# Optimization experiments

Hardware: AMD Instinct MI355X
Metric: run time of the kernel (lower is better)

## Reference

```python
import jax, jax.numpy as jnp
import numpy as np

HIDDEN = 128
IN_SIZE = 1
OUT_SIZE = 1
ENC_T = 8192
DEC_T = 4096


def _lstm_step(h, c, x, Wih, Whh, bih, bhh):
    # PyTorch LSTM gate order: i, f, g, o
    gates = Wih @ x + Whh @ h + bih + bhh  # [4H]
    i, f, g, o = jnp.split(gates, 4)
    c = jax.nn.sigmoid(f) * c + jax.nn.sigmoid(i) * jnp.tanh(g)
    h = jax.nn.sigmoid(o) * jnp.tanh(c)
    return h, c


def setup_inputs() -> dict:
    key = jax.random.key(0)
    ks = jax.random.split(key, 12)
    k = 1.0 / np.sqrt(HIDDEN)  # PyTorch default init bound
    u = lambda kk, shape: jax.random.uniform(kk, shape, jnp.float32, -k, k)
    return {
        "input_seq": jax.random.normal(ks[0], (ENC_T,), jnp.float32),
        "enc_Wih": u(ks[1], (4 * HIDDEN, IN_SIZE)),
        "enc_Whh": u(ks[2], (4 * HIDDEN, HIDDEN)),
        "enc_bih": u(ks[3], (4 * HIDDEN,)),
        "enc_bhh": u(ks[4], (4 * HIDDEN,)),
        "dec_Wih": u(ks[5], (4 * HIDDEN, OUT_SIZE)),
        "dec_Whh": u(ks[6], (4 * HIDDEN, HIDDEN)),
        "dec_bih": u(ks[7], (4 * HIDDEN,)),
        "dec_bhh": u(ks[8], (4 * HIDDEN,)),
        "fc_W": u(ks[9], (OUT_SIZE, HIDDEN)),
        "fc_b": u(ks[10], (OUT_SIZE,)),
        "target_seq_len": DEC_T,
    }


def reference(input_seq, enc_Wih, enc_Whh, enc_bih, enc_bhh,
              dec_Wih, dec_Whh, dec_bih, dec_bhh, fc_W, fc_b,
              target_seq_len):
    H = enc_Whh.shape[1]
    dt = input_seq.dtype

    def enc_step(carry, xt):
        h, c = carry
        h, c = _lstm_step(h, c, xt[None], enc_Wih, enc_Whh, enc_bih, enc_bhh)
        return (h, c), None

    (h, c), _ = jax.lax.scan(enc_step,
                             (jnp.zeros(H, dt), jnp.zeros(H, dt)),
                             input_seq)

    def dec_step(carry, _):
        h, c, y = carry  # y: previous prediction, shape [1]
        h, c = _lstm_step(h, c, y, dec_Wih, dec_Whh, dec_bih, dec_bhh)
        pred = fc_W @ h + fc_b  # [1]
        return (h, c, pred), pred

    _, preds = jax.lax.scan(dec_step, (h, c, jnp.zeros(1, dt)),
                            None, length=target_seq_len)
    # preds: [T_out, 1] -> torch.cat(outputs, dim=1) gives [1, T_out]
    return preds.T
```

## Files before the change

### kernel.cpp

```cpp
#include <hip/hip_runtime.h>


#define H      128
#define ENC_T  8192
#define DEC_T  4096
#define NT     512
#define NBLK   1
#define PBUF   5120

#define LOG2E  1.4426950408889634f

typedef float v2f __attribute__((ext_vector_type(2)));

__device__ __forceinline__ v2f pk_fma_s(v2f a, v2f b_sgpr, v2f c) {
    v2f d;
    asm("v_pk_fma_f32 %0, %1, %2, %3" : "=v"(d) : "v"(a), "s"(b_sgpr), "v"(c));
    return d;
}
__device__ __forceinline__ v2f pk_mul_s(v2f a, v2f b_sgpr) {
    v2f d;
    asm("v_pk_mul_f32 %0, %1, %2" : "=v"(d) : "v"(a), "s"(b_sgpr));
    return d;
}
__device__ __forceinline__ v2f pk_fma(v2f a, v2f b, v2f c) {
    v2f d;
    asm("v_pk_fma_f32 %0, %1, %2, %3" : "=v"(d) : "v"(a), "v"(b), "v"(c));
    return d;
}
__device__ __forceinline__ float exp2fast(float x) {
    float d;
    asm("v_exp_f32 %0, %1" : "=v"(d) : "v"(x));
    return d;
}
__device__ __forceinline__ float tanhfast(float x) {
    const float e = exp2fast(2.0f * LOG2E * x);
    return fmaf(-2.0f, __builtin_amdgcn_rcpf(1.0f + e), 1.0f);
}
__device__ __forceinline__ float rdlane(float v, int l) {
    return __int_as_float(__builtin_amdgcn_readlane(__float_as_int(v), l));
}
template <int CTRL>
__device__ __forceinline__ float qperm(float v) {
    return __int_as_float(
        __builtin_amdgcn_mov_dpp(__float_as_int(v), CTRL, 0xf, 0xf, true));
}

__global__ __launch_bounds__(NT, 2)
void seq2seq_lstm(const float* __restrict__ input_seq,
                  const float* __restrict__ enc_Wih,
                  const float* __restrict__ enc_Whh,
                  const float* __restrict__ enc_bih,
                  const float* __restrict__ enc_bhh,
                  const float* __restrict__ dec_Wih,
                  const float* __restrict__ dec_Whh,
                  const float* __restrict__ dec_bih,
                  const float* __restrict__ dec_bhh,
                  const float* __restrict__ fc_W,
                  const float* __restrict__ fc_b,
                  float* __restrict__ out,
                  unsigned* __restrict__ wsflag)
{
    (void)wsflag;
    __shared__ __align__(16) float xin[ENC_T];
    __shared__ __align__(16) float hbuf[2][H];
    __shared__ __align__(16) float part[2][PBUF];

    const int t    = threadIdx.x;
    const int lane = t & 63;
    const int wv   = t >> 6;
    const int jb   = 16 * wv;
    const int qq   = lane >> 2;
    const int g    = lane & 3;
    const int myu  = jb + qq;
    const int myrow = g * H + myu;

    const int rbase = 80 * wv + 16 * g + qq;
    const int wbase = 640 * wv + 80 * (lane >> 4) + (lane & 15);

    const float sA  = (g == 2) ? 1.0f : 0.0f;
    const float sB  = (g == 2) ? -2.0f : 1.0f;
    const float sS2 = ((g == 2) ? 2.0f : -1.0f) * LOG2E;

    {
        const float4* s = (const float4*)input_seq;
        float4* d = (float4*)xin;
        for (int i = t; i < ENC_T / 4; i += NT) d[i] = s[i];
    }

    v2f w2[8][8];
#pragma unroll
    for (int s = 0; s < 8; ++s) {
        const v2f* Wr = (const v2f*)(enc_Whh + (64 * s + lane) * H + jb);
#pragma unroll
        for (int jj = 0; jj < 8; ++jj) w2[s][jj] = Wr[jj];
    }
    float bias_r = enc_bih[myrow] + enc_bhh[myrow];
    float wih_r  = enc_Wih[myrow];

    float cst = 0.f;
    float hn  = 0.f;
    __syncthreads();

#define MATVEC(PB)                                                          \
    {                                                                       \
        v2f acc2[8];                                                        \
        {                          \
            const float se = rdlane(hn, 3);                                 \
            const float so = rdlane(hn, 7);                                 \
            const v2f hp = {se, so};                                        \
            _Pragma("unroll") for (int s = 0; s < 8; ++s)                   \
                acc2[s] = pk_mul_s(w2[s][0], hp);                           \
        }                                                                   \
        _Pragma("unroll") for (int jj = 1; jj < 8; ++jj) {                  \
            const float se = rdlane(hn, 8 * jj + 3);                        \
            const float so = rdlane(hn, 8 * jj + 7);                        \
            const v2f hp = {se, so};                                        \
            _Pragma("unroll") for (int s = 0; s < 8; ++s)                   \
                acc2[s] = pk_fma_s(w2[s][jj], hp, acc2[s]);                 \
        }                                                                   \
        float* pb_ = &part[PB][wbase];                                      \
        pb_[0]   = acc2[0].x + acc2[0].y;                                   \
        pb_[320] = acc2[1].x + acc2[1].y;                                   \
        pb_[16]  = acc2[2].x + acc2[2].y;                                   \
        pb_[336] = acc2[3].x + acc2[3].y;                                   \
        pb_[32]  = acc2[4].x + acc2[4].y;                                   \
        pb_[352] = acc2[5].x + acc2[5].y;                                   \
        pb_[48]  = acc2[6].x + acc2[6].y;                                   \
        pb_[368] = acc2[7].x + acc2[7].y;                                   \
    }

#define RED_LOAD(PB)                                                        \
    const float* rb_ = &part[PB][rbase];                                    \
    const float r0_ = rb_[0],    r1_ = rb_[640],  r2_ = rb_[1280],          \
                r3_ = rb_[1920], r4_ = rb_[2560], r5_ = rb_[3200],          \
                r6_ = rb_[3840], r7_ = rb_[4480];

#define RED_FIN(PB, ABASE, STH)                                             \
    {                                                                       \
        const float a = (ABASE) + (((r0_ + r1_) + (r2_ + r3_)) +            \
                                   ((r4_ + r5_) + (r6_ + r7_)));            \
        const float e = exp2fast(sS2 * a);                                  \
        const float r = __builtin_amdgcn_rcpf(1.0f + e);                    \
        const float v = fmaf(sB, r, sA);                                    \
        const float vi = qperm<0x00>(v);                   \
        const float vf = qperm<0x55>(v);                   \
        const float vg = qperm<0xAA>(v);                   \
        const float vo = qperm<0xFF>(v);                   \
        cst = fmaf(vf, cst, vi * vg);                                       \
        hn  = vo * tanhfast(cst);                                           \
        if (STH && g == 3) hbuf[PB][myu] = hn;                              \
    }

#define OUTBLK(ST, HB)                                                      \
    if (wv == 7 && (ST) >= 1) {                                             \
        float p = fmaf(fwl, hbuf[HB][lane], fwh * hbuf[HB][64 + lane]);     \
        p += qperm<0xB1>(p);                                     \
        p += qperm<0x4E>(p);                                     \
        _Pragma("unroll") for (int m = 32; m >= 4; m >>= 1)                 \
            p += __shfl_xor(p, m, 64);                                      \
        if (lane == 0) out[(ST) - 1] = p + fcb;                             \
    }

    for (int st = 0; st < ENC_T; st += 2) {
        const float2 xx = *(const float2*)&xin[st];
        {
            MATVEC(0);
            __syncthreads();
            RED_LOAD(0);
            RED_FIN(0, fmaf(wih_r, xx.x, bias_r), 0);
        }
        {
            MATVEC(1);
            __syncthreads();
            RED_LOAD(1);
            RED_FIN(1, fmaf(wih_r, xx.y, bias_r), 0);
        }
    }
    if (g == 3) hbuf[1][myu] = hn;

    const float fcb = fc_b[0];
    const float fwl = fc_W[lane];
    const float fwh = fc_W[64 + lane];
#pragma unroll
    for (int s = 0; s < 8; ++s) {
        const int r = 64 * s + lane;
        const float vi = dec_Wih[r];
        const v2f vip = {vi, vi};
        const v2f* Wr = (const v2f*)(dec_Whh + r * H + jb);
        const v2f* Fr = (const v2f*)(fc_W + jb);
#pragma unroll
        for (int jj = 0; jj < 8; ++jj)
            w2[s][jj] = pk_fma(vip, Fr[jj], Wr[jj]);
    }
    wih_r  = dec_Wih[myrow];
    bias_r = dec_bih[myrow] + dec_bhh[myrow] + wih_r * fcb;
    __syncthreads();
    float q0;
    {
        float p = fmaf(fwl, hbuf[1][lane], fwh * hbuf[1][64 + lane]);
        p += qperm<0xB1>(p);
        p += qperm<0x4E>(p);
#pragma unroll
        for (int m = 32; m >= 4; m >>= 1) p += __shfl_xor(p, m, 64);
        q0 = p + fcb;
    }
    float cb = bias_r - wih_r * q0;

    for (int st = 0; st < DEC_T; st += 2) {
        {
            MATVEC(0);
            __syncthreads();
            RED_LOAD(0);
            OUTBLK(st, 1);
            RED_FIN(0, cb, 1);
            cb = bias_r;
        }
        {
            MATVEC(1);
            __syncthreads();
            RED_LOAD(1);
            OUTBLK(st + 1, 0);
            RED_FIN(1, cb, 1);
        }
    }

    __syncthreads();
    if (wv == 7) {
        float p = fmaf(fwl, hbuf[1][lane], fwh * hbuf[1][64 + lane]);
        p += qperm<0xB1>(p);
        p += qperm<0x4E>(p);
#pragma unroll
        for (int m = 32; m >= 4; m >>= 1) p += __shfl_xor(p, m, 64);
        if (lane == 0) out[DEC_T - 1] = p + fcb;
    }
}

extern "C" void kernel_launch(void* const* d_in, const int* in_sizes, int n_in,
                              void* d_out, int out_size, void* d_ws, size_t ws_size,
                              hipStream_t stream)
{
    (void)in_sizes; (void)n_in; (void)ws_size; (void)out_size;
    seq2seq_lstm<<<NBLK, NT, 0, stream>>>(
        (const float*)d_in[0],
        (const float*)d_in[1],
        (const float*)d_in[2],
        (const float*)d_in[3],
        (const float*)d_in[4],
        (const float*)d_in[5],
        (const float*)d_in[6],
        (const float*)d_in[7],
        (const float*)d_in[8],
        (const float*)d_in[9],
        (const float*)d_in[10],
        (float*)d_out,
        (unsigned*)d_ws);
}
```

Baseline: 7.505 ms.

## Split LSTM recurrence across 4 waves instead of 8 with 2 gates per lane

Halves the block from 8 to 4 wavefronts. Each wave now owns 32 hidden columns, holding 16 v2f weights per row-slot, and each lane finishes two gate rows. Lane pairs then exchange values through a DPP swap instead of a 4-lane quad permute. The aim is a cheaper __syncthreads barrier and a smaller cross-wave reduction, since the shared partial-sum buffer shrinks. In exchange each wave does twice the matvec FMAs per step and needs about twice the weight registers, which lowers occupancy and lengthens the per-step critical path.

```diff
diff --git a/kernel.cpp b/kernel.cpp
--- a/kernel.cpp
+++ b/kernel.cpp
@@ -4,9 +4,9 @@
 #define H      128
 #define ENC_T  8192
 #define DEC_T  4096
-#define NT     512
+#define NT     256
 #define NBLK   1
-#define PBUF   5120
+#define PBUF   2048
 
 #define LOG2E  1.4426950408889634f
 
@@ -45,7 +45,7 @@
         __builtin_amdgcn_mov_dpp(__float_as_int(v), CTRL, 0xf, 0xf, true));
 }
 
-__global__ __launch_bounds__(NT, 2)
+__global__ __launch_bounds__(NT, 1)
 void seq2seq_lstm(const float* __restrict__ input_seq,
                   const float* __restrict__ enc_Wih,
                   const float* __restrict__ enc_Whh,
@@ -68,18 +68,16 @@
     const int t    = threadIdx.x;
     const int lane = t & 63;
     const int wv   = t >> 6;
-    const int jb   = 16 * wv;
-    const int qq   = lane >> 2;
-    const int g    = lane & 3;
-    const int myu  = jb + qq;
-    const int myrow = g * H + myu;
-
-    const int rbase = 80 * wv + 16 * g + qq;
-    const int wbase = 640 * wv + 80 * (lane >> 4) + (lane & 15);
-
-    const float sA  = (g == 2) ? 1.0f : 0.0f;
-    const float sB  = (g == 2) ? -2.0f : 1.0f;
-    const float sS2 = ((g == 2) ? 2.0f : -1.0f) * LOG2E;
+    const int jb   = 32 * wv;
+    const int u    = jb + (lane >> 1);
+    const bool ev  = (lane & 1) == 0;
+    const int r0   = 128 * (lane & 1) + u;
+    const int r1   = r0 + 256;
+    const int wbase = 512 * wv + lane;
+
+    const float sA  = ev ? 1.0f : 0.0f;
+    const float sB  = ev ? -2.0f : 1.0f;
+    const float sS2 = (ev ? 2.0f : -1.0f) * LOG2E;
 
     {
         const float4* s = (const float4*)input_seq;
@@ -87,15 +85,17 @@
         for (int i = t; i < ENC_T / 4; i += NT) d[i] = s[i];
     }
 
-    v2f w2[8][8];
+    v2f w2[8][16];
 #pragma unroll
     for (int s = 0; s < 8; ++s) {
         const v2f* Wr = (const v2f*)(enc_Whh + (64 * s + lane) * H + jb);
 #pragma unroll
-        for (int jj = 0; jj < 8; ++jj) w2[s][jj] = Wr[jj];
-    }
-    float bias_r = enc_bih[myrow] + enc_bhh[myrow];
-    float wih_r  = enc_Wih[myrow];
+        for (int jj = 0; jj < 16; ++jj) w2[s][jj] = Wr[jj];
+    }
+    float bias0 = enc_bih[r0] + enc_bhh[r0];
+    float bias1 = enc_bih[r1] + enc_bhh[r1];
+    float wih0  = enc_Wih[r0];
+    float wih1  = enc_Wih[r1];
 
     float cst = 0.f;
     float hn  = 0.f;
@@ -105,54 +105,52 @@
     {                                                                       \
         v2f acc2[8];                                                        \
         {                          \
-            const float se = rdlane(hn, 3);                                 \
-            const float so = rdlane(hn, 7);                                 \
+            const float se = rdlane(hn, 0);                                 \
+            const float so = rdlane(hn, 2);                                 \
             const v2f hp = {se, so};                                        \
             _Pragma("unroll") for (int s = 0; s < 8; ++s)                   \
                 acc2[s] = pk_mul_s(w2[s][0], hp);                           \
         }                                                                   \
-        _Pragma("unroll") for (int jj = 1; jj < 8; ++jj) {                  \
-            const float se = rdlane(hn, 8 * jj + 3);                        \
-            const float so = rdlane(hn, 8 * jj + 7);                        \
+        _Pragma("unroll") for (int jj = 1; jj < 16; ++jj) {                 \
+            const float se = rdlane(hn, 4 * jj);                            \
+            const float so = rdlane(hn, 4 * jj + 2);                        \
             const v2f hp = {se, so};                                        \
             _Pragma("unroll") for (int s = 0; s < 8; ++s)                   \
                 acc2[s] = pk_fma_s(w2[s][jj], hp, acc2[s]);                 \
         }                                                                   \
         float* pb_ = &part[PB][wbase];                                      \
-        pb_[0]   = acc2[0].x + acc2[0].y;                                   \
-        pb_[320] = acc2[1].x + acc2[1].y;                                   \
-        pb_[16]  = acc2[2].x + acc2[2].y;                                   \
-        pb_[336] = acc2[3].x + acc2[3].y;                                   \
-        pb_[32]  = acc2[4].x + acc2[4].y;                                   \
-        pb_[352] = acc2[5].x + acc2[5].y;                                   \
-        pb_[48]  = acc2[6].x + acc2[6].y;                                   \
-        pb_[368] = acc2[7].x + acc2[7].y;                                   \
+        _Pragma("unroll") for (int s = 0; s < 8; ++s)                       \
+            pb_[64 * s] = acc2[s].x + acc2[s].y;                            \
     }
 
 #define RED_LOAD(PB)                                                        \
-    const float* rb_ = &part[PB][rbase];                                    \
-    const float r0_ = rb_[0],    r1_ = rb_[640],  r2_ = rb_[1280],          \
-                r3_ = rb_[1920], r4_ = rb_[2560], r5_ = rb_[3200],          \
-                r6_ = rb_[3840], r7_ = rb_[4480];
-
-#define RED_FIN(PB, ABASE, STH)                                             \
+    const float* rb_ = &part[PB][r0];                                       \
+    const float p00_ = rb_[0],    p01_ = rb_[512],                          \
+                p02_ = rb_[1024], p03_ = rb_[1536];                         \
+    const float p10_ = rb_[256],  p11_ = rb_[768],                          \
+                p12_ = rb_[1280], p13_ = rb_[1792];
+
+#define RED_FIN(PB, AB0, AB1, STH)                                          \
     {                                                                       \
-        const float a = (ABASE) + (((r0_ + r1_) + (r2_ + r3_)) +            \
-                                   ((r4_ + r5_) + (r6_ + r7_)));            \
-        const float e = exp2fast(sS2 * a);                                  \
-        const float r = __builtin_amdgcn_rcpf(1.0f + e);                    \
-        const float v = fmaf(sB, r, sA);                                    \
-        const float vi = qperm<0x00>(v);                   \
-        const float vf = qperm<0x55>(v);                   \
-        const float vg = qperm<0xAA>(v);                   \
-        const float vo = qperm<0xFF>(v);                   \
+        const float a0 = (AB0) + ((p00_ + p01_) + (p02_ + p03_));           \
+        const float a1 = (AB1) + ((p10_ + p11_) + (p12_ + p13_));           \
+        const float e0 = exp2fast(-LOG2E * a0);                             \
+        const float v0 = __builtin_amdgcn_rcpf(1.0f + e0);     \
+        const float e1 = exp2fast(sS2 * a1);                                \
+        const float v1 = fmaf(sB, __builtin_amdgcn_rcpf(1.0f + e1), sA);    \
+        const float s0_ = qperm<0xB1>(v0);                   \
+        const float s1_ = qperm<0xB1>(v1);                                  \
+        const float vi = ev ? v0  : s0_;                                    \
+        const float vf = ev ? s0_ : v0;                                     \
+        const float vg = ev ? v1  : s1_;                                    \
+        const float vo = ev ? s1_ : v1;                                     \
         cst = fmaf(vf, cst, vi * vg);                                       \
         hn  = vo * tanhfast(cst);                                           \
-        if (STH && g == 3) hbuf[PB][myu] = hn;                              \
+        if (STH && ev) hbuf[PB][u] = hn;                                    \
     }
 
 #define OUTBLK(ST, HB)                                                      \
-    if (wv == 7 && (ST) >= 1) {                                             \
+    if (wv == 3 && (ST) >= 1) {                                             \
         float p = fmaf(fwl, hbuf[HB][lane], fwh * hbuf[HB][64 + lane]);     \
         p += qperm<0xB1>(p);                                     \
         p += qperm<0x4E>(p);                                     \
@@ -167,16 +165,16 @@
             MATVEC(0);
             __syncthreads();
             RED_LOAD(0);
-            RED_FIN(0, fmaf(wih_r, xx.x, bias_r), 0);
+            RED_FIN(0, fmaf(wih0, xx.x, bias0), fmaf(wih1, xx.x, bias1), 0);
         }
         {
             MATVEC(1);
             __syncthreads();
             RED_LOAD(1);
-            RED_FIN(1, fmaf(wih_r, xx.y, bias_r), 0);
-        }
-    }
-    if (g == 3) hbuf[1][myu] = hn;
+            RED_FIN(1, fmaf(wih0, xx.y, bias0), fmaf(wih1, xx.y, bias1), 0);
+        }
+    }
+    if (ev) hbuf[1][u] = hn;
 
     const float fcb = fc_b[0];
     const float fwl = fc_W[lane];
@@ -184,16 +182,18 @@
 #pragma unroll
     for (int s = 0; s < 8; ++s) {
         const int r = 64 * s + lane;
-        const float vi = dec_Wih[r];
-        const v2f vip = {vi, vi};
+        const float viw = dec_Wih[r];
+        const v2f vip = {viw, viw};
         const v2f* Wr = (const v2f*)(dec_Whh + r * H + jb);
         const v2f* Fr = (const v2f*)(fc_W + jb);
 #pragma unroll
-        for (int jj = 0; jj < 8; ++jj)
+        for (int jj = 0; jj < 16; ++jj)
             w2[s][jj] = pk_fma(vip, Fr[jj], Wr[jj]);
     }
-    wih_r  = dec_Wih[myrow];
-    bias_r = dec_bih[myrow] + dec_bhh[myrow] + wih_r * fcb;
+    wih0  = dec_Wih[r0];
+    wih1  = dec_Wih[r1];
+    bias0 = dec_bih[r0] + dec_bhh[r0] + wih0 * fcb;
+    bias1 = dec_bih[r1] + dec_bhh[r1] + wih1 * fcb;
     __syncthreads();
     float q0;
     {
@@ -204,7 +204,8 @@
         for (int m = 32; m >= 4; m >>= 1) p += __shfl_xor(p, m, 64);
         q0 = p + fcb;
     }
-    float cb = bias_r - wih_r * q0;
+    float cb0 = bias0 - wih0 * q0;
+    float cb1 = bias1 - wih1 * q0;
 
     for (int st = 0; st < DEC_T; st += 2) {
         {
@@ -212,20 +213,20 @@
             __syncthreads();
             RED_LOAD(0);
             OUTBLK(st, 1);
-            RED_FIN(0, cb, 1);
-            cb = bias_r;
+            RED_FIN(0, cb0, cb1, 1);
+            cb0 = bias0; cb1 = bias1;
         }
         {
             MATVEC(1);
             __syncthreads();
             RED_LOAD(1);
             OUTBLK(st + 1, 0);
-            RED_FIN(1, cb, 1);
+            RED_FIN(1, cb0, cb1, 1);
         }
     }
 
     __syncthreads();
-    if (wv == 7) {
+    if (wv == 3) {
         float p = fmaf(fwl, hbuf[1][lane], fwh * hbuf[1][64 + lane]);
         p += qperm<0xB1>(p);
         p += qperm<0x4E>(p);
```

Result: slower. 11.91 ms (+58.7%).
